# Kernel tuning notes

Measured on AMD Instinct MI355X. Metric: run time of the kernel, lower is better.

## Reference

```python
import jax, jax.numpy as jnp
import numpy as np

LEAK = 0.9
BASE_THRESH = 1.0
BN_EPS = 1e-5

@jax.custom_vjp
def spike_fn(x):
    return (x >= 0).astype(x.dtype)

def _spike_fwd(x):
    return (x >= 0).astype(x.dtype), x

def _spike_bwd(x, g):
    return (g / (1.0 + 5.0 * jnp.abs(x)) ** 2,)

spike_fn.defvjp(_spike_fwd, _spike_bwd)


def setup_inputs() -> dict:
    key = jax.random.key(0)
    ks = jax.random.split(key, 8)
    B, T, C, H, NC, DT = 256, 2048, 64, 64, 4, 50
    kin_spikes_seq = jax.random.normal(ks[0], (B, T, C), dtype=jnp.float32)
    tda_features = jax.random.normal(ks[1], (B, DT), dtype=jnp.float32)
    # spatial_conv1x1: Linear(64 -> 64, bias=False); weight [out, in]
    W_spatial = jax.random.normal(ks[2], (H, C), dtype=jnp.float32) / np.sqrt(C)
    bn_gamma = jnp.ones((H,), dtype=jnp.float32)
    bn_beta = jnp.zeros((H,), dtype=jnp.float32)
    # class_conv1x1: Linear(64 -> 4, bias=False)
    W_class = jax.random.normal(ks[3], (NC, H), dtype=jnp.float32) / np.sqrt(H)
    lateral = jnp.eye(NC, dtype=jnp.float32) * 0.8 - 0.1
    # tda_to_thresh: Linear(50 -> 4)
    W_tda = jax.random.normal(ks[4], (NC, DT), dtype=jnp.float32) / np.sqrt(DT)
    b_tda = jnp.zeros((NC,), dtype=jnp.float32)
    return {
        "kin_spikes_seq": kin_spikes_seq,
        "tda_features": tda_features,
        "W_spatial": W_spatial,
        "bn_gamma": bn_gamma,
        "bn_beta": bn_beta,
        "W_class": W_class,
        "lateral": lateral,
        "W_tda": W_tda,
        "b_tda": b_tda,
    }


def reference(kin_spikes_seq, tda_features, W_spatial, bn_gamma, bn_beta,
              W_class, lateral, W_tda, b_tda):
    # [B, T, C] @ [C, H] -> [B, T, H]
    x_proj = jnp.einsum("btc,hc->bth", kin_spikes_seq, W_spatial)
    # BatchNorm1d in training mode: per-channel stats over (B, T)
    mean = jnp.mean(x_proj, axis=(0, 1))
    var = jnp.var(x_proj, axis=(0, 1))
    x_proj = (x_proj - mean) * jax.lax.rsqrt(var + BN_EPS) * bn_gamma + bn_beta

    tda_mod = jax.nn.sigmoid(tda_features @ W_tda.T + b_tda) * 0.5  # [B, 4]
    dynamic_thresh = BASE_THRESH + tda_mod

    B = kin_spikes_seq.shape[0]
    H, NC = W_class.shape[1], W_class.shape[0]
    mem1 = jnp.zeros((B, H), dtype=x_proj.dtype)
    mem2 = jnp.zeros((B, NC), dtype=x_proj.dtype)
    spike_sum = jnp.zeros((B, NC), dtype=x_proj.dtype)

    def step(carry, xt):
        mem1, mem2, ssum = carry
        mem1 = LEAK * mem1 + xt
        spk1 = spike_fn(mem1 - BASE_THRESH)
        mem1 = mem1 * (1.0 - spk1)
        cur2 = (spk1 @ W_class.T) @ lateral  # [B, 4]
        mem2 = LEAK * mem2 + cur2
        spk2 = spike_fn(mem2 - dynamic_thresh)
        mem2 = mem2 * (1.0 - spk2)
        return (mem1, mem2, ssum + spk2), None

    xs = jnp.swapaxes(x_proj, 0, 1)  # [T, B, H]
    (mem1, mem2, spike_sum), _ = jax.lax.scan(step, (mem1, mem2, spike_sum), xs)
    return spike_sum
```

## Files before the change

kernel.cpp:

```cpp
#include <hip/hip_runtime.h>
#include <cstdint>
#include <cstddef>
#include <cmath>

#define BB 256
#define TB 2048
#define NROWS (BB*TB)
#define R1 256
#define NBLK_K1 (NROWS/R1)
#define NBLK1 4096

typedef float f32x4 __attribute__((ext_vector_type(4)));
typedef float f32x2 __attribute__((ext_vector_type(2)));

#define OFF_X      0ull
#define SZ_X       ((size_t)NROWS*64*4)
#define OFF_PART   (OFF_X + SZ_X)
#define SZ_PART    ((size_t)128*NBLK1*4)
#define OFF_STAT   (OFF_PART + SZ_PART)
#define SZ_STAT    (128*8)

__global__ __launch_bounds__(256, 2) void k1_gemm(const float* __restrict__ kin,
                                                  const float* __restrict__ Wsp,
                                                  float* __restrict__ xproj,
                                                  float* __restrict__ partials) {
  __shared__ float4 As[R1 * 16];
  __shared__ f32x4 Wp[32 * 32];
  const int tid = threadIdx.x;
  const int ty = tid >> 3;
  const int tx = tid & 7;
  const size_t r0 = (size_t)blockIdx.x * R1;

  const f32x4* kin4 = (const f32x4*)(kin + r0 * 64);
  #pragma unroll
  for (int k = 0; k < 16; ++k) {
    int idx = k * 256 + tid;
    int r = idx >> 4, cc = idx & 15;
    f32x4 v = __builtin_nontemporal_load(&kin4[idx]);
    As[r * 16 + (cc ^ ((r >> 3) & 7))] = make_float4(v.x, v.y, v.z, v.w);
  }
  #pragma unroll
  for (int k = 0; k < 4; ++k) {
    int idx = k * 256 + tid;
    int p = idx >> 5, q = idx & 31;
    float2 w0 = *(const float2*)(Wsp + (2 * p) * 64 + 2 * q);
    float2 w1 = *(const float2*)(Wsp + (2 * p + 1) * 64 + 2 * q);
    Wp[p * 32 + (q ^ ((p >> 2) & 7))] = (f32x4){w0.x, w1.x, w0.y, w1.y};
  }
  __syncthreads();

  f32x2 acc2[8][4];
  #pragma unroll
  for (int i = 0; i < 8; ++i)
    #pragma unroll
    for (int jp = 0; jp < 4; ++jp) acc2[i][jp] = (f32x2){0.f, 0.f};

  #pragma unroll 1
  for (int cc = 0; cc < 16; ++cc) {
    float4 av[8];
    f32x4 q0[4], q1[4];
    #pragma unroll
    for (int i = 0; i < 8; ++i)
      av[i] = As[(8 * ty + i) * 16 + (cc ^ (ty & 7))];
    #pragma unroll
    for (int jp = 0; jp < 4; ++jp) {
      const int p = 4 * tx + jp;
      q0[jp] = Wp[p * 32 + ((2 * cc)     ^ tx)];
      q1[jp] = Wp[p * 32 + ((2 * cc + 1) ^ tx)];
    }
    #pragma unroll
    for (int i = 0; i < 8; ++i) {
      #pragma unroll
      for (int jp = 0; jp < 4; ++jp) {
        acc2[i][jp] = __builtin_elementwise_fma((f32x2){av[i].x, av[i].x}, q0[jp].xy, acc2[i][jp]);
        acc2[i][jp] = __builtin_elementwise_fma((f32x2){av[i].y, av[i].y}, q0[jp].zw, acc2[i][jp]);
        acc2[i][jp] = __builtin_elementwise_fma((f32x2){av[i].z, av[i].z}, q1[jp].xy, acc2[i][jp]);
        acc2[i][jp] = __builtin_elementwise_fma((f32x2){av[i].w, av[i].w}, q1[jp].zw, acc2[i][jp]);
      }
    }
  }

  #pragma unroll
  for (int i = 0; i < 8; ++i) {
    const size_t row = r0 + 8 * ty + i;
    f32x4 lo = {acc2[i][0].x, acc2[i][0].y, acc2[i][1].x, acc2[i][1].y};
    f32x4 hi = {acc2[i][2].x, acc2[i][2].y, acc2[i][3].x, acc2[i][3].y};
    *(f32x4*)(xproj + row * 64 + 8 * tx)     = lo;
    *(f32x4*)(xproj + row * 64 + 8 * tx + 4) = hi;
  }

  __syncthreads();
  float* Sm = (float*)As;
  float* Sq = Sm + 64 * 33;
  #pragma unroll
  for (int j = 0; j < 8; ++j) {
    const int col = 8 * tx + j;
    float s = 0.f, q = 0.f;
    #pragma unroll
    for (int i = 0; i < 8; ++i) {
      float v = (j & 1) ? acc2[i][j >> 1].y : acc2[i][j >> 1].x;
      s += v;
      q += v * v;
    }
    Sm[col * 33 + ty] = s;
    Sq[col * 33 + ty] = q;
  }
  __syncthreads();
  if (tid < 64) {
    float s0 = 0.f, q0 = 0.f, s1 = 0.f, q1 = 0.f;
    #pragma unroll
    for (int g = 0; g < 16; ++g)  { s0 += Sm[tid * 33 + g]; q0 += Sq[tid * 33 + g]; }
    #pragma unroll
    for (int g = 16; g < 32; ++g) { s1 += Sm[tid * 33 + g]; q1 += Sq[tid * 33 + g]; }
    const size_t p0 = 2 * (size_t)blockIdx.x;
    partials[(size_t)tid * NBLK1 + p0]            = s0;
    partials[(size_t)tid * NBLK1 + p0 + 1]        = s1;
    partials[(size_t)(64 + tid) * NBLK1 + p0]     = q0;
    partials[(size_t)(64 + tid) * NBLK1 + p0 + 1] = q1;
  }
}

__global__ __launch_bounds__(256) void k2a_reduce(const float* __restrict__ partials,
                                                  double* __restrict__ statd) {
  __shared__ double sd[256];
  const int idx = blockIdx.x;
  double acc = 0.0;
  for (int k = threadIdx.x; k < NBLK1; k += 256)
    acc += (double)partials[(size_t)idx * NBLK1 + k];
  sd[threadIdx.x] = acc;
  __syncthreads();
  for (int s = 128; s > 0; s >>= 1) {
    if (threadIdx.x < s) sd[threadIdx.x] += sd[threadIdx.x + s];
    __syncthreads();
  }
  if (threadIdx.x == 0) statd[idx] = sd[0];
}

#define XSW 68
#define K45_LOAD(BUF, TBASE)                                             \
  { _Pragma("unroll") for (int k_ = 0; k_ < 16; ++k_) {                  \
      f32x4 v = *(const f32x4*)(cr + (TBASE) + 4 * k_);                  \
      BUF[4 * k_] = v.x; BUF[4 * k_ + 1] = v.y;                          \
      BUF[4 * k_ + 2] = v.z; BUF[4 * k_ + 3] = v.w; } }

#define K45_CHUNK(CUR, NXT0)                                  \
  { _Pragma("unroll") for (int i_ = 0; i_ < 64; ++i_) {       \
      bool sp = (mem2 >= th);                                 \
      cnt += sp ? 1u : 0u;                                    \
      float xn = (i_ < 63) ? CUR[(i_ + 1) & 63] : (NXT0);     \
      mem2 = sp ? xn : fmaf(mem2, 0.9f, xn);                  \
    } }

#define PROD_WRITE(BF)                                                        \
  { _Pragma("unroll") for (int h2 = 0; h2 < 64; ++h2) {                       \
      float pv;                                                               \
      switch (h2 & 3) {                                                       \
        case 0: pv = pregs[h2 >> 2].x; break;                                 \
        case 1: pv = pregs[h2 >> 2].y; break;                                 \
        case 2: pv = pregs[h2 >> 2].z; break;                                 \
        default: pv = pregs[h2 >> 2].w; break;                                \
      }                                                                       \
      pv = fmaf(pv, scL[h2], shL[h2]);                                        \
      xs[BF][h2][lane] = pv;                                                  \
    } }

#define PROD_ISSUE(C)                                                         \
  { const f32x4* xr_ = (const f32x4*)(xproj + ((size_t)b * TB +               \
                                      (size_t)(C) * 64 + lane) * 64);         \
    _Pragma("unroll") for (int k_ = 0; k_ < 16; ++k_) pregs[k_] = xr_[k_]; }

__global__ __launch_bounds__(256) void k345_scan(const float* __restrict__ xproj,
                                                 const double* __restrict__ statd,
                                                 const float* __restrict__ gamma,
                                                 const float* __restrict__ beta,
                                                 const float* __restrict__ Wc,
                                                 const float* __restrict__ lat,
                                                 const float* __restrict__ tda,
                                                 const float* __restrict__ Wtda,
                                                 const float* __restrict__ btda,
                                                 float* __restrict__ out) {
  __shared__ float xs[4][64][XSW];
  __shared__ unsigned long long masksT[TB];
  __shared__ unsigned long long masksL[TB];
  __shared__ float WcL[256];
  __shared__ float latL[16];
  __shared__ float thL[4];
  __shared__ float scL[64];
  __shared__ float shL[64];
  __shared__ float lbuf[4][TB + 4];
  const int tid = threadIdx.x, b = blockIdx.x;
  const int lane = tid & 63;
  const int wv = tid >> 6;

  WcL[tid] = Wc[tid];
  if (tid < 16) latL[tid] = lat[tid];

  float mem = 0.f;
  f32x4 pregs[16];

  if (wv == 0) {
    const int h = lane;
    const double mean = statd[h] / (double)NROWS;
    const double ex2  = statd[64 + h] / (double)NROWS;
    const double var  = ex2 - mean * mean;
    const double scd  = (double)gamma[h] / sqrt(var + 1e-5);
    scL[h] = (float)scd;
    shL[h] = (float)((double)beta[h] - mean * scd);
  } else if (wv == 3) {
    if (lane < 4) {
      const int j = lane;
      double acc = (double)btda[j];
      for (int k = 0; k < 50; ++k)
        acc += (double)tda[b * 50 + k] * (double)Wtda[j * 50 + k];
      double sig = 1.0 / (1.0 + exp(-acc));
      thL[j] = (float)(1.0 + 0.5 * sig);
    }
  } else {
    PROD_ISSUE(wv - 1)
  }
  __syncthreads();

  if (wv == 1) { PROD_WRITE(0) PROD_ISSUE(3) }
  else if (wv == 2) { PROD_WRITE(1) }
  else if (wv == 3) { PROD_ISSUE(2) }
  __syncthreads();

  if (wv == 0) {
    mem = xs[0][lane][0];
  }

  #pragma unroll 1
  for (int n = 0; n < 32; ++n) {
    if (n + 2 < 32 && wv == 1 + ((n + 2) % 3)) {
      const int bf = (n + 2) & 3;
      PROD_WRITE(bf)
    }
    if (n + 4 < 32 && wv == 1 + ((n + 1) % 3)) {
      PROD_ISSUE(n + 4)
    }
    if (wv == 0) {
      const int bf = n & 3;
      const f32x4* xrow = (const f32x4*)&xs[bf][lane][0];
      f32x4 av[16];
      #pragma unroll
      for (int i = 0; i < 16; ++i) av[i] = xrow[i];
      const float nxt0 = (n < 31) ? xs[(n + 1) & 3][lane][0] : 0.f;
      unsigned keepLo = 0u, keepHi = 0u;
      #pragma unroll
      for (int i_ = 0; i_ < 64; ++i_) {
        bool sp = (mem >= 1.0f);
        if (i_ < 32) { unsigned t2 = keepLo | (1u << i_);        keepLo = sp ? t2 : keepLo; }
        else         { unsigned t2 = keepHi | (1u << (i_ - 32)); keepHi = sp ? t2 : keepHi; }
        float xn = (i_ < 63) ? av[(i_ + 1) >> 2][(i_ + 1) & 3] : nxt0;
        mem = sp ? xn : fmaf(mem, 0.9f, xn);
      }
      masksT[n * 64 + lane] = ((unsigned long long)keepHi << 32) | keepLo;
    }
    asm volatile("s_waitcnt lgkmcnt(0)" ::: "memory");
    __builtin_amdgcn_sched_barrier(0);
    __builtin_amdgcn_s_barrier();
  }
  __syncthreads();

  #pragma unroll 1
  for (int cc2 = 0; cc2 < 8; ++cc2) {
    const int chunk = wv * 8 + cc2;
    const unsigned long long m = masksT[chunk * 64 + lane];
    const unsigned mlo = (unsigned)m, mhi = (unsigned)(m >> 32);
    unsigned long long keep = 0ull;
    #pragma unroll
    for (int tb = 0; tb < 64; ++tb) {
      bool sp = (((tb < 32) ? (mlo >> tb) : (mhi >> (tb - 32))) & 1u) != 0u;
      unsigned long long mb = __ballot(sp);
      if (lane == tb) keep = mb;
    }
    masksL[chunk * 64 + lane] = keep;
  }
  __syncthreads();

  #pragma unroll 1
  for (int c = 0; c < 8; ++c) {
    const int t = c * 256 + tid;
    const unsigned long long m = masksL[t];
    const unsigned lo = (unsigned)m, hi = (unsigned)(m >> 32);
    float v0 = 0.f, v1 = 0.f, v2 = 0.f, v3 = 0.f;
    #pragma unroll
    for (int hh = 0; hh < 32; ++hh) {
      const float bit = (float)((lo >> hh) & 1u);
      v0 = fmaf(bit, WcL[hh],       v0);
      v1 = fmaf(bit, WcL[64 + hh],  v1);
      v2 = fmaf(bit, WcL[128 + hh], v2);
      v3 = fmaf(bit, WcL[192 + hh], v3);
    }
    #pragma unroll
    for (int hh = 32; hh < 64; ++hh) {
      const float bit = (float)((hi >> (hh - 32)) & 1u);
      v0 = fmaf(bit, WcL[hh],       v0);
      v1 = fmaf(bit, WcL[64 + hh],  v1);
      v2 = fmaf(bit, WcL[128 + hh], v2);
      v3 = fmaf(bit, WcL[192 + hh], v3);
    }
    { float cx = v0 * latL[0];  cx = fmaf(v1, latL[4],  cx); cx = fmaf(v2, latL[8],  cx); cx = fmaf(v3, latL[12], cx); lbuf[0][t] = cx; }
    { float cx = v0 * latL[1];  cx = fmaf(v1, latL[5],  cx); cx = fmaf(v2, latL[9],  cx); cx = fmaf(v3, latL[13], cx); lbuf[1][t] = cx; }
    { float cx = v0 * latL[2];  cx = fmaf(v1, latL[6],  cx); cx = fmaf(v2, latL[10], cx); cx = fmaf(v3, latL[14], cx); lbuf[2][t] = cx; }
    { float cx = v0 * latL[3];  cx = fmaf(v1, latL[7],  cx); cx = fmaf(v2, latL[11], cx); cx = fmaf(v3, latL[15], cx); lbuf[3][t] = cx; }
  }
  __syncthreads();
  if (tid >= 64) return;

  const int j4 = tid & 3;
  const float th = thL[j4];
  const float* cr = lbuf[j4];
  float ca[64], cb[64];

  K45_LOAD(ca, 0)
  float mem2 = ca[0];
  unsigned cnt = 0;

  #pragma unroll 1
  for (int t0 = 0; t0 < TB; t0 += 128) {
    K45_LOAD(cb, t0 + 64)
    K45_CHUNK(ca, cb[0])
    if (t0 + 128 < TB) { K45_LOAD(ca, t0 + 128) }
    K45_CHUNK(cb, ca[0])
  }
  if (tid < 4) out[b * 4 + j4] = (float)cnt;
}

extern "C" void kernel_launch(void* const* d_in, const int* in_sizes, int n_in,
                              void* d_out, int out_size, void* d_ws, size_t ws_size,
                              hipStream_t stream) {
  const float* kin   = (const float*)d_in[0];
  const float* tda   = (const float*)d_in[1];
  const float* Wsp   = (const float*)d_in[2];
  const float* gamma = (const float*)d_in[3];
  const float* beta  = (const float*)d_in[4];
  const float* Wc    = (const float*)d_in[5];
  const float* lat   = (const float*)d_in[6];
  const float* Wtda  = (const float*)d_in[7];
  const float* btda  = (const float*)d_in[8];

  char* ws = (char*)d_ws;
  float*  xproj    = (float*)(ws + OFF_X);
  float*  partials = (float*)(ws + OFF_PART);
  double* statd    = (double*)(ws + OFF_STAT);
  float*  out      = (float*)d_out;

  k1_gemm  <<<dim3(NBLK_K1), dim3(256), 0, stream>>>(kin, Wsp, xproj, partials);
  k2a_reduce<<<dim3(128),  dim3(256), 0, stream>>>(partials, statd);
  k345_scan<<<dim3(BB),    dim3(256), 0, stream>>>(xproj, statd, gamma, beta,
                                                   Wc, lat, tda, Wtda, btda, out);
}
```

Before: 148.6 us.

## Parallelize layer-1 LIF scan speculatively across time chunks with merge fixup

Replaces the single-wave sequential layer-1 membrane scan, which was fed by producer waves through an LDS ring buffer, with a speculative parallel scan. Eight waves (512 threads) each scan two 128-step time chunks starting from a reset state and record spike masks and end states. A single wave then re-scans each chunk from the true state and stops early once the trajectory hits a spike that the speculation also hit, since both paths then coincide. This aims to shorten the serial critical path but adds redundant global loads and a data-dependent fixup pass whose length depends on when trajectories converge.

```diff
diff --git a/kernel.cpp b/kernel.cpp
--- a/kernel.cpp
+++ b/kernel.cpp
@@ -12,6 +12,7 @@
 
 typedef float f32x4 __attribute__((ext_vector_type(4)));
 typedef float f32x2 __attribute__((ext_vector_type(2)));
+typedef unsigned long long u64;
 
 #define OFF_X      0ull
 #define SZ_X       ((size_t)NROWS*64*4)
@@ -136,7 +137,6 @@
   if (threadIdx.x == 0) statd[idx] = sd[0];
 }
 
-#define XSW 68
 #define K45_LOAD(BUF, TBASE)                                             \
   { _Pragma("unroll") for (int k_ = 0; k_ < 16; ++k_) {                  \
       f32x4 v = *(const f32x4*)(cr + (TBASE) + 4 * k_);                  \
@@ -151,25 +151,7 @@
       mem2 = sp ? xn : fmaf(mem2, 0.9f, xn);                  \
     } }
 
-#define PROD_WRITE(BF)                                                        \
-  { _Pragma("unroll") for (int h2 = 0; h2 < 64; ++h2) {                       \
-      float pv;                                                               \
-      switch (h2 & 3) {                                                       \
-        case 0: pv = pregs[h2 >> 2].x; break;                                 \
-        case 1: pv = pregs[h2 >> 2].y; break;                                 \
-        case 2: pv = pregs[h2 >> 2].z; break;                                 \
-        default: pv = pregs[h2 >> 2].w; break;                                \
-      }                                                                       \
-      pv = fmaf(pv, scL[h2], shL[h2]);                                        \
-      xs[BF][h2][lane] = pv;                                                  \
-    } }
-
-#define PROD_ISSUE(C)                                                         \
-  { const f32x4* xr_ = (const f32x4*)(xproj + ((size_t)b * TB +               \
-                                      (size_t)(C) * 64 + lane) * 64);         \
-    _Pragma("unroll") for (int k_ = 0; k_ < 16; ++k_) pregs[k_] = xr_[k_]; }
-
-__global__ __launch_bounds__(256) void k345_scan(const float* __restrict__ xproj,
+__global__ __launch_bounds__(512) void k345_scan(const float* __restrict__ xproj,
                                                  const double* __restrict__ statd,
                                                  const float* __restrict__ gamma,
                                                  const float* __restrict__ beta,
@@ -179,9 +161,9 @@
                                                  const float* __restrict__ Wtda,
                                                  const float* __restrict__ btda,
                                                  float* __restrict__ out) {
-  __shared__ float xs[4][64][XSW];
-  __shared__ unsigned long long masksT[TB];
-  __shared__ unsigned long long masksL[TB];
+  __shared__ u64 masksT[TB];
+  __shared__ u64 masksL[TB];
+  __shared__ float specEndL[16 * 64];
   __shared__ float WcL[256];
   __shared__ float latL[16];
   __shared__ float thL[4];
@@ -192,11 +174,8 @@
   const int lane = tid & 63;
   const int wv = tid >> 6;
 
-  WcL[tid] = Wc[tid];
+  if (tid < 256) WcL[tid] = Wc[tid];
   if (tid < 16) latL[tid] = lat[tid];
-
-  float mem = 0.f;
-  f32x4 pregs[16];
 
   if (wv == 0) {
     const int h = lane;
@@ -206,72 +185,149 @@
     const double scd  = (double)gamma[h] / sqrt(var + 1e-5);
     scL[h] = (float)scd;
     shL[h] = (float)((double)beta[h] - mean * scd);
-  } else if (wv == 3) {
-    if (lane < 4) {
-      const int j = lane;
-      double acc = (double)btda[j];
-      for (int k = 0; k < 50; ++k)
-        acc += (double)tda[b * 50 + k] * (double)Wtda[j * 50 + k];
-      double sig = 1.0 / (1.0 + exp(-acc));
-      thL[j] = (float)(1.0 + 0.5 * sig);
-    }
-  } else {
-    PROD_ISSUE(wv - 1)
-  }
-  __syncthreads();
-
-  if (wv == 1) { PROD_WRITE(0) PROD_ISSUE(3) }
-  else if (wv == 2) { PROD_WRITE(1) }
-  else if (wv == 3) { PROD_ISSUE(2) }
+  } else if (wv == 7 && lane < 4) {
+    const int j = lane;
+    double acc = (double)btda[j];
+    for (int k = 0; k < 50; ++k)
+      acc += (double)tda[b * 50 + k] * (double)Wtda[j * 50 + k];
+    double sig = 1.0 / (1.0 + exp(-acc));
+    thL[j] = (float)(1.0 + 0.5 * sig);
+  }
+  __syncthreads();
+
+  const float sc = scL[lane], sh = shL[lane];
+  const float* xb = xproj + (size_t)b * TB * 64 + lane;
+
+  {
+    float sa[64], sb[64];
+    #pragma unroll 1
+    for (int rep = 0; rep < 2; ++rep) {
+      const int cs = wv + rep * 8;
+      const int t0 = cs * 128;
+      #pragma unroll
+      for (int i = 0; i < 64; ++i) sa[i] = xb[(size_t)(t0 + i) * 64];
+      #pragma unroll
+      for (int i = 0; i < 64; ++i) sb[i] = xb[(size_t)(t0 + 64 + i) * 64];
+      const float nxtraw = (cs < 15) ? xb[(size_t)(t0 + 128) * 64] : 0.f;
+
+      float mem = fmaf(sa[0], sc, sh);
+      unsigned l0 = 0u, h0 = 0u, l1 = 0u, h1 = 0u;
+      #pragma unroll
+      for (int i = 0; i < 64; ++i) {
+        bool sp = (mem >= 1.0f);
+        if (i < 32) { unsigned t2 = l0 | (1u << i);        l0 = sp ? t2 : l0; }
+        else        { unsigned t2 = h0 | (1u << (i - 32)); h0 = sp ? t2 : h0; }
+        float rn = (i < 63) ? sa[i + 1] : sb[0];
+        float xn = fmaf(rn, sc, sh);
+        mem = sp ? xn : fmaf(mem, 0.9f, xn);
+      }
+      #pragma unroll
+      for (int i = 0; i < 64; ++i) {
+        bool sp = (mem >= 1.0f);
+        if (i < 32) { unsigned t2 = l1 | (1u << i);        l1 = sp ? t2 : l1; }
+        else        { unsigned t2 = h1 | (1u << (i - 32)); h1 = sp ? t2 : h1; }
+        float rn = (i < 63) ? sb[i + 1] : nxtraw;
+        float xn = fmaf(rn, sc, sh);
+        mem = sp ? xn : fmaf(mem, 0.9f, xn);
+      }
+      masksT[(2 * cs) * 64 + lane]     = ((u64)h0 << 32) | l0;
+      masksT[(2 * cs + 1) * 64 + lane] = ((u64)h1 << 32) | l1;
+      specEndL[cs * 64 + lane] = mem;
+    }
+  }
   __syncthreads();
 
   if (wv == 0) {
-    mem = xs[0][lane][0];
-  }
+    float pa[65], pb[65];
+    #pragma unroll
+    for (int i = 0; i < 65; ++i) pa[i] = xb[(size_t)i * 64];
+    float memv = fmaf(pa[0], sc, sh);
+
+    #pragma unroll 1
+    for (int c = 0; c < 16; ++c) {
+      if (c < 15) {
+        #pragma unroll
+        for (int i = 0; i < 65; ++i) pb[i] = xb[(size_t)((c + 1) * 128 + i) * 64];
+      }
+      const u64 mt0 = masksT[(2 * c) * 64 + lane];
+      const u64 mt1 = masksT[(2 * c + 1) * 64 + lane];
+      const unsigned mt0lo = (unsigned)mt0, mt0hi = (unsigned)(mt0 >> 32);
+      const unsigned mt1lo = (unsigned)mt1, mt1hi = (unsigned)(mt1 >> 32);
+      bool merged = false;
+      int mstep = 128;
+      unsigned e0lo = 0u, e0hi = 0u, e1lo = 0u, e1hi = 0u;
+
+      #pragma unroll 1
+      for (int g = 0; g < 8; ++g) {
+        #pragma unroll
+        for (int k = 0; k < 8; ++k) {
+          const int i = g * 8 + k;
+          bool act = !merged;
+          bool sp = act && (memv >= 1.0f);
+          if (i < 32) { unsigned t2 = e0lo | (1u << i);        e0lo = sp ? t2 : e0lo; }
+          else        { unsigned t2 = e0hi | (1u << (i - 32)); e0hi = sp ? t2 : e0hi; }
+          bool specbit = (((i < 32) ? (mt0lo >> i) : (mt0hi >> (i - 32))) & 1u) != 0u;
+          bool co = sp && specbit;
+          mstep = co ? i : mstep;
+          merged = merged || co;
+          float rn = (i < 63) ? pa[i + 1] : pa[64];
+          float xn = fmaf(rn, sc, sh);
+          float upd = sp ? xn : fmaf(memv, 0.9f, xn);
+          memv = (act && !co) ? upd : memv;
+        }
+        if (__all((int)merged)) break;
+      }
+
+      if (!__all((int)merged)) {
+        #pragma unroll
+        for (int j = 0; j < 63; ++j) pa[j] = xb[(size_t)(c * 128 + 65 + j) * 64];
+        #pragma unroll
+        for (int i = 64; i < 128; ++i) {
+          bool act = !merged;
+          bool sp = act && (memv >= 1.0f);
+          const int i2 = i - 64;
+          if (i2 < 32) { unsigned t2 = e1lo | (1u << i2);        e1lo = sp ? t2 : e1lo; }
+          else         { unsigned t2 = e1hi | (1u << (i2 - 32)); e1hi = sp ? t2 : e1hi; }
+          bool specbit = (((i2 < 32) ? (mt1lo >> i2) : (mt1hi >> (i2 - 32))) & 1u) != 0u;
+          bool co = sp && specbit;
+          mstep = co ? i : mstep;
+          merged = merged || co;
+          float rn = (i < 127) ? pa[i - 64] : ((c < 15) ? pb[0] : 0.f);
+          float xn = fmaf(rn, sc, sh);
+          float upd = sp ? xn : fmaf(memv, 0.9f, xn);
+          memv = (act && !co) ? upd : memv;
+        }
+      }
+
+      const u64 ex0 = ((u64)e0hi << 32) | e0lo;
+      const u64 ex1 = ((u64)e1hi << 32) | e1lo;
+      const bool m1 = merged && (mstep < 64);
+      const bool m2 = merged && (mstep >= 64);
+      const u64 lm = (2ull << (mstep & 63)) - 1ull;
+      const u64 f0 = m1 ? ((ex0 & lm) | (mt0 & ~lm)) : ex0;
+      const u64 f1 = m1 ? mt1 : (m2 ? ((ex1 & lm) | (mt1 & ~lm)) : ex1);
+      masksT[(2 * c) * 64 + lane]     = f0;
+      masksT[(2 * c + 1) * 64 + lane] = f1;
+      memv = merged ? specEndL[c * 64 + lane] : memv;
+
+      if (c < 15) {
+        #pragma unroll
+        for (int i = 0; i < 65; ++i) pa[i] = pb[i];
+      }
+    }
+  }
+  __syncthreads();
 
   #pragma unroll 1
-  for (int n = 0; n < 32; ++n) {
-    if (n + 2 < 32 && wv == 1 + ((n + 2) % 3)) {
-      const int bf = (n + 2) & 3;
-      PROD_WRITE(bf)
-    }
-    if (n + 4 < 32 && wv == 1 + ((n + 1) % 3)) {
-      PROD_ISSUE(n + 4)
-    }
-    if (wv == 0) {
-      const int bf = n & 3;
-      const f32x4* xrow = (const f32x4*)&xs[bf][lane][0];
-      f32x4 av[16];
-      #pragma unroll
-      for (int i = 0; i < 16; ++i) av[i] = xrow[i];
-      const float nxt0 = (n < 31) ? xs[(n + 1) & 3][lane][0] : 0.f;
-      unsigned keepLo = 0u, keepHi = 0u;
-      #pragma unroll
-      for (int i_ = 0; i_ < 64; ++i_) {
-        bool sp = (mem >= 1.0f);
-        if (i_ < 32) { unsigned t2 = keepLo | (1u << i_);        keepLo = sp ? t2 : keepLo; }
-        else         { unsigned t2 = keepHi | (1u << (i_ - 32)); keepHi = sp ? t2 : keepHi; }
-        float xn = (i_ < 63) ? av[(i_ + 1) >> 2][(i_ + 1) & 3] : nxt0;
-        mem = sp ? xn : fmaf(mem, 0.9f, xn);
-      }
-      masksT[n * 64 + lane] = ((unsigned long long)keepHi << 32) | keepLo;
-    }
-    asm volatile("s_waitcnt lgkmcnt(0)" ::: "memory");
-    __builtin_amdgcn_sched_barrier(0);
-    __builtin_amdgcn_s_barrier();
-  }
-  __syncthreads();
-
-  #pragma unroll 1
-  for (int cc2 = 0; cc2 < 8; ++cc2) {
-    const int chunk = wv * 8 + cc2;
-    const unsigned long long m = masksT[chunk * 64 + lane];
+  for (int cc2 = 0; cc2 < 4; ++cc2) {
+    const int chunk = wv * 4 + cc2;
+    const u64 m = masksT[chunk * 64 + lane];
     const unsigned mlo = (unsigned)m, mhi = (unsigned)(m >> 32);
-    unsigned long long keep = 0ull;
+    u64 keep = 0ull;
     #pragma unroll
     for (int tb = 0; tb < 64; ++tb) {
       bool sp = (((tb < 32) ? (mlo >> tb) : (mhi >> (tb - 32))) & 1u) != 0u;
-      unsigned long long mb = __ballot(sp);
+      u64 mb = __ballot(sp);
       if (lane == tb) keep = mb;
     }
     masksL[chunk * 64 + lane] = keep;
@@ -279,9 +335,9 @@
   __syncthreads();
 
   #pragma unroll 1
-  for (int c = 0; c < 8; ++c) {
-    const int t = c * 256 + tid;
-    const unsigned long long m = masksL[t];
+  for (int c = 0; c < 4; ++c) {
+    const int t = c * 512 + tid;
+    const u64 m = masksL[t];
     const unsigned lo = (unsigned)m, hi = (unsigned)(m >> 32);
     float v0 = 0.f, v1 = 0.f, v2 = 0.f, v3 = 0.f;
     #pragma unroll
@@ -348,6 +404,6 @@
 
   k1_gemm  <<<dim3(NBLK_K1), dim3(256), 0, stream>>>(kin, Wsp, xproj, partials);
   k2a_reduce<<<dim3(128),  dim3(256), 0, stream>>>(partials, statd);
-  k345_scan<<<dim3(BB),    dim3(256), 0, stream>>>(xproj, statd, gamma, beta,
+  k345_scan<<<dim3(BB),    dim3(512), 0, stream>>>(xproj, statd, gamma, beta,
                                                    Wc, lat, tda, Wtda, btda, out);
 }
```

After: 359.8 us. 2.42x slower.
